# Kernel tuning notes

Measured on AMD Instinct MI355X. Metric: run time of the kernel, lower is better.

The kernel has to match this reference:

```python
import jax, jax.numpy as jnp
import numpy as np

DIM, DSTATE, DCONV, DTRANK = 192, 16, 4, 12
BSZ, HH, WW = 2, 64, 64
DW = DIM * 2  # SGFN dw_dim


def _silu(x):
    return x * jax.nn.sigmoid(x)


def _mamba(u, in_w, conv_w, conv_b, xproj_w, dt_w, dt_b, A_log, Dp, out_w):
    # u: [B, L, d_model]; d_inner == d_model (expand=1)
    Bb, L, d = u.shape
    xz = jnp.einsum('bld,ed->ble', u, in_w)            # [B,L,2d]
    xm, z = jnp.split(xz, 2, axis=-1)
    # causal depthwise conv1d (pad left d_conv-1, truncate to L)
    xt = xm.transpose(0, 2, 1)                          # [B,d,L]
    xt = jax.lax.conv_general_dilated(
        xt, conv_w[:, None, :], (1,), [(DCONV - 1, 0)],
        feature_group_count=d, dimension_numbers=('NCH', 'OIH', 'NCH'))
    xm = _silu((xt + conv_b[:, None]).transpose(0, 2, 1))  # [B,L,d]
    x_dbl = jnp.einsum('bld,ed->ble', xm, xproj_w)      # [B,L,r+2N]
    dt, Bm, Cm = jnp.split(x_dbl, [DTRANK, DTRANK + DSTATE], axis=-1)
    dt = jax.nn.softplus(jnp.einsum('blr,dr->bld', dt, dt_w) + dt_b)  # [B,L,d]
    A = -jnp.exp(A_log)                                 # [d,N]
    dA = jnp.exp(dt[..., None] * A)                     # [B,L,d,N]
    dBu = dt[..., None] * Bm[:, :, None, :] * xm[..., None]  # [B,L,d,N]

    def step(h, inp):
        a, bu, c = inp
        h = a * h + bu                                  # [B,d,N]
        return h, jnp.einsum('bdn,bn->bd', h, c)

    h0 = jnp.zeros((Bb, d, DSTATE), u.dtype)
    _, ys = jax.lax.scan(step, h0, (dA.swapaxes(0, 1), dBu.swapaxes(0, 1), Cm.swapaxes(0, 1)))
    y = ys.swapaxes(0, 1) + Dp * xm                     # [B,L,d]
    y = y * _silu(z)
    return jnp.einsum('bld,ed->ble', y, out_w)


def _forward(x, ln_w, ln_b,
             in_w0, conv_w0, conv_b0, xproj_w0, dt_w0, dt_b0, A_log0, D0, out_w0,
             in_w1, conv_w1, conv_b1, xproj_w1, dt_w1, dt_b1, A_log1, D1, out_w1,
             scale_mod, c1w, c1b, dww, dwb, c2w, c2b, gamma):
    Bb, C, Hh, Wh = x.shape
    # LayerNorm over channel dim (applied in BHWC layout)
    xn = x.transpose(0, 2, 3, 1)
    mu = xn.mean(-1, keepdims=True)
    var = ((xn - mu) ** 2).mean(-1, keepdims=True)
    xn = (xn - mu) * jax.lax.rsqrt(var + 1e-5) * ln_w + ln_b
    # MHSS: bidirectional Mamba over flattened spatial sequence
    xf = xn.reshape(Bb, Hh * Wh, C)
    out = _mamba(xf, in_w0, conv_w0, conv_b0, xproj_w0, dt_w0, dt_b0, A_log0, D0, out_w0)
    out = out + _mamba(xf[:, ::-1], in_w1, conv_w1, conv_b1, xproj_w1, dt_w1, dt_b1, A_log1, D1, out_w1)[:, ::-1]
    xm = out.reshape(Bb, Hh, Wh, C).transpose(0, 3, 1, 2) * scale_mod
    # SGFN
    t = jnp.einsum('bchw,oc->bohw', xm, c1w) + c1b[:, None, None]
    t = jax.lax.conv_general_dilated(
        t, dww, (1, 1), [(1, 1), (1, 1)],
        feature_group_count=dww.shape[0],
        dimension_numbers=('NCHW', 'OIHW', 'NCHW')) + dwb[:, None, None]
    t1, t2 = jnp.split(t, 2, axis=1)
    sg = jnp.einsum('bchw,oc->bohw', t1 * jax.nn.sigmoid(t2), c2w) + c2b[:, None, None]
    return x + gamma * (xm + sg)


def _mamba_params(key):
    ks = jax.random.split(key, 6)
    d, s = DIM, 0.02
    dt = jnp.exp(jax.random.uniform(ks[4], (d,), minval=np.log(1e-3), maxval=np.log(1e-1)))
    return dict(
        in_w=jax.random.normal(ks[0], (2 * d, d)) * s,
        conv_w=jax.random.normal(ks[1], (d, DCONV)) * s,
        conv_b=jnp.zeros((d,)),
        xproj_w=jax.random.normal(ks[2], (DTRANK + 2 * DSTATE, d)) * s,
        dt_w=jax.random.normal(ks[3], (d, DTRANK)) * (DTRANK ** -0.5),
        dt_b=jnp.log(jnp.expm1(dt)),  # inverse softplus
        A_log=jnp.log(jnp.tile(jnp.arange(1, DSTATE + 1, dtype=jnp.float32), (d, 1))),
        D=jnp.ones((d,)),
        out_w=jax.random.normal(ks[5], (d, d)) * s,
    )


def setup_inputs() -> dict:
    key = jax.random.key(0)
    ks = jax.random.split(key, 8)
    p0 = _mamba_params(ks[1])
    p1 = _mamba_params(ks[2])
    s = 0.02
    inp = {
        'x': jax.random.normal(ks[0], (BSZ, DIM, HH, WW), jnp.float32),
        'ln_w': jnp.ones((DIM,)),
        'ln_b': jnp.zeros((DIM,)),
        'scale_mod': jnp.full((1,), 0.25),
        'c1w': jax.random.normal(ks[3], (2 * DW, DIM)) * s,
        'c1b': jnp.zeros((2 * DW,)),
        'dww': jax.random.normal(ks[4], (2 * DW, 1, 3, 3)) * s,
        'dwb': jnp.zeros((2 * DW,)),
        'c2w': jax.random.normal(ks[5], (DIM, DW)) * s,
        'c2b': jnp.zeros((DIM,)),
        'gamma': jnp.full((1,), 0.1),  # nonzero so the block is non-trivial
    }
    for name, p in (('0', p0), ('1', p1)):
        inp['in_w' + name] = p['in_w']
        inp['conv_w' + name] = p['conv_w']
        inp['conv_b' + name] = p['conv_b']
        inp['xproj_w' + name] = p['xproj_w']
        inp['dt_w' + name] = p['dt_w']
        inp['dt_b' + name] = p['dt_b']
        inp['A_log' + name] = p['A_log']
        inp['D' + name] = p['D']
        inp['out_w' + name] = p['out_w']
    return inp


def reference(x, ln_w, ln_b,
              in_w0, conv_w0, conv_b0, xproj_w0, dt_w0, dt_b0, A_log0, D0, out_w0,
              in_w1, conv_w1, conv_b1, xproj_w1, dt_w1, dt_b1, A_log1, D1, out_w1,
              scale_mod, c1w, c1b, dww, dwb, c2w, c2b, gamma):
    return _forward(x, ln_w, ln_b,
                    in_w0, conv_w0, conv_b0, xproj_w0, dt_w0, dt_b0, A_log0, D0, out_w0,
                    in_w1, conv_w1, conv_b1, xproj_w1, dt_w1, dt_b1, A_log1, D1, out_w1,
                    scale_mod, c1w, c1b, dww, dwb, c2w, c2b, gamma)
```

## Files before the change

kernel.cpp:

```cpp
#include <hip/hip_runtime.h>
#include <hip/hip_bf16.h>

#define BSZ   2
#define SEQL  4096
#define BLR   8192
#define DM    192
#define NST   16
#define DTR   12
#define XDW   44
#define XDP   48
#define NCH   128
#define CT    32

typedef float f32x4 __attribute__((ext_vector_type(4)));
typedef __bf16 bf16x8 __attribute__((ext_vector_type(8)));
typedef __bf16 bf16x4 __attribute__((ext_vector_type(4)));

__device__ __forceinline__ float sigf(float x) { return 1.f / (1.f + __expf(-x)); }
__device__ __forceinline__ float siluf(float x) { return x * sigf(x); }
__device__ __forceinline__ float softplusf(float x) { return x > 20.f ? x : log1pf(__expf(x)); }

__global__ __launch_bounds__(256) void ln_kernel(const float* __restrict__ x,
                                                 const float* __restrict__ lw,
                                                 const float* __restrict__ lb,
                                                 __bf16* __restrict__ xn) {
    __shared__ float Xs[192][68];
    __shared__ float Rs[4][64], Rq[4][64];
    __shared__ float Mu[64], Rv[64];
    const int tid = threadIdx.x;
    const int blk = blockIdx.x;
    const int b = blk >> 6;
    const int hw0 = (blk & 63) << 6;
    {
        int i4 = tid & 15, cp = tid >> 4;
        for (int c = cp; c < 192; c += 16) {
            float4 v = *reinterpret_cast<const float4*>(x + ((size_t)b * DM + c) * 4096 + hw0 + i4 * 4);
            *reinterpret_cast<float4*>(&Xs[c][i4 * 4]) = v;
        }
    }
    __syncthreads();
    const int i = tid & 63, part = tid >> 6;
    float s = 0.f, q = 0.f;
    for (int c = part * 48; c < part * 48 + 48; c++) {
        float v = Xs[c][i];
        s += v; q += v * v;
    }
    Rs[part][i] = s; Rq[part][i] = q;
    __syncthreads();
    if (part == 0) {
        float ss = Rs[0][i] + Rs[1][i] + Rs[2][i] + Rs[3][i];
        float qq = Rq[0][i] + Rq[1][i] + Rq[2][i] + Rq[3][i];
        float mu = ss * (1.f / DM);
        float var = qq * (1.f / DM) - mu * mu;
        Mu[i] = mu; Rv[i] = rsqrtf(var + 1e-5f);
    }
    __syncthreads();
    float mu = Mu[i], rs = Rv[i];
    size_t rowb = ((size_t)b * 4096 + hw0 + i) * DM;
#pragma unroll
    for (int j = 0; j < 6; j++) {
        int c0 = part * 48 + j * 8;
        bf16x8 o;
#pragma unroll
        for (int e = 0; e < 8; e++) {
            int c = c0 + e;
            o[e] = (__bf16)((Xs[c][i] - mu) * rs * lw[c] + lb[c]);
        }
        *reinterpret_cast<bf16x8*>(xn + rowb + c0) = o;
    }
}

template <int EPI>
__global__ __launch_bounds__(256) void gemm_mfma(const __bf16* __restrict__ A, int lda,
                                                 const __bf16* __restrict__ W, int ldw,
                                                 __bf16* __restrict__ C, int ldc,
                                                 int N, int K,
                                                 const float* __restrict__ bias,
                                                 const float* __restrict__ scal,
                                                 const __bf16* __restrict__ aux,
                                                 const float* __restrict__ xres,
                                                 float* __restrict__ outp) {
    __shared__ __bf16 As[64][40];
    __shared__ __bf16 Ws[64][40];
    const int tid  = threadIdx.x;
    const int wave = tid >> 6, lane = tid & 63;
    const int ko = lane >> 4, lm = lane & 15;
    const int wm = (wave & 1) * 32, wn = (wave >> 1) * 32;
    const int m0 = blockIdx.y << 6;
    int n0 = blockIdx.x << 6;
    if (EPI == 5) {
        int dir = blockIdx.x;
        A += dir * DM;
        W += (size_t)dir * XDW * DM;
        C += (size_t)dir * BLR * XDP;
        n0 = 0;
    }
    const int r = tid >> 2, cq = (tid & 3) * 8;
    f32x4 acc[2][2] = {};

    for (int k0 = 0; k0 < K; k0 += 32) {
        {
            bf16x8 pk;
            const __bf16* ap = A + (size_t)(m0 + r) * lda + k0 + cq;
            if (k0 + cq + 8 <= K) pk = *reinterpret_cast<const bf16x8*>(ap);
            else {
#pragma unroll
                for (int j = 0; j < 8; j++) pk[j] = (k0 + cq + j < K) ? ap[j] : (__bf16)0.f;
            }
            *reinterpret_cast<bf16x8*>(&As[r][cq]) = pk;
        }
        {
            bf16x8 pk = {};
            if (n0 + r < N) {
                const __bf16* wp = W + (size_t)(n0 + r) * ldw + k0 + cq;
                if (k0 + cq + 8 <= K) pk = *reinterpret_cast<const bf16x8*>(wp);
                else {
#pragma unroll
                    for (int j = 0; j < 8; j++) pk[j] = (k0 + cq + j < K) ? wp[j] : (__bf16)0.f;
                }
            }
            *reinterpret_cast<bf16x8*>(&Ws[r][cq]) = pk;
        }
        __syncthreads();
        bf16x8 af[2], bfr[2];
#pragma unroll
        for (int ti = 0; ti < 2; ti++)
            af[ti] = *reinterpret_cast<bf16x8*>(&As[wm + ti * 16 + lm][ko * 8]);
#pragma unroll
        for (int tj = 0; tj < 2; tj++)
            bfr[tj] = *reinterpret_cast<bf16x8*>(&Ws[wn + tj * 16 + lm][ko * 8]);
#pragma unroll
        for (int ti = 0; ti < 2; ti++)
#pragma unroll
            for (int tj = 0; tj < 2; tj++)
                acc[ti][tj] = __builtin_amdgcn_mfma_f32_16x16x32_bf16(af[ti], bfr[tj], acc[ti][tj], 0, 0, 0);
        __syncthreads();
    }

    if constexpr (EPI == 4) {
        __shared__ float Cs[64][65];
#pragma unroll
        for (int ti = 0; ti < 2; ti++)
#pragma unroll
            for (int tj = 0; tj < 2; tj++) {
                int nn = n0 + wn + tj * 16 + lm;
#pragma unroll
                for (int reg = 0; reg < 4; reg++) {
                    int m = m0 + wm + ti * 16 + ko * 4 + reg;
                    float v = acc[ti][tj][reg];
                    if (nn < N) v += (float)aux[(size_t)m * DM + nn];
                    Cs[wm + ti * 16 + ko * 4 + reg][wn + tj * 16 + lm] = v;
                }
            }
        __syncthreads();
        float g = scal[0];
#pragma unroll
        for (int rep = 0; rep < 16; rep++) {
            int idx = rep * 256 + tid;
            int n = idx >> 6, mi = idx & 63;
            int nn = n0 + n;
            if (nn >= N) continue;
            int m = m0 + mi;
            int b = m >> 12, hw = m & 4095;
            size_t oi = (((size_t)b * DM + nn) << 12) + hw;
            outp[oi] = xres[oi] + g * (Cs[mi][n] + bias[nn]);
        }
        return;
    }

#pragma unroll
    for (int ti = 0; ti < 2; ti++)
#pragma unroll
        for (int tj = 0; tj < 2; tj++) {
            int n = n0 + wn + tj * 16 + lm;
            if (n >= N) continue;
#pragma unroll
            for (int reg = 0; reg < 4; reg++) {
                int m = m0 + wm + ti * 16 + ko * 4 + reg;
                float v = acc[ti][tj][reg];
                if (EPI == 1) v += bias[n];
                if (EPI == 3) v *= scal[0];
                C[(size_t)m * ldc + n] = (__bf16)v;
            }
        }
}

__global__ __launch_bounds__(256) void conv_silu_kernel(const __bf16* __restrict__ xz,
                                                        const float* __restrict__ cwt,
                                                        const float* __restrict__ cbcat,
                                                        __bf16* __restrict__ xc) {
    int idx = blockIdx.x * 256 + threadIdx.x;
    int colq = (idx % 48) << 3;
    int row = idx / 48;
    int dir = colq >= DM;
    int b = row >> 12, l = row & 4095;
    int xoff = colq + dir * DM;
    float acc[8];
    {
        float4 b0 = *reinterpret_cast<const float4*>(cbcat + colq);
        float4 b1 = *reinterpret_cast<const float4*>(cbcat + colq + 4);
        acc[0] = b0.x; acc[1] = b0.y; acc[2] = b0.z; acc[3] = b0.w;
        acc[4] = b1.x; acc[5] = b1.y; acc[6] = b1.z; acc[7] = b1.w;
    }
#pragma unroll
    for (int k = 0; k < 4; k++) {
        int ls = dir ? (l + 3 - k) : (l - 3 + k);
        if (ls < 0 || ls >= SEQL) continue;
        bf16x8 xv = *reinterpret_cast<const bf16x8*>(xz + ((size_t)(b << 12) + ls) * 768 + xoff);
        const float* wv = cwt + k * 384 + colq;
#pragma unroll
        for (int e = 0; e < 8; e++) acc[e] += wv[e] * (float)xv[e];
    }
    bf16x8 o;
#pragma unroll
    for (int e = 0; e < 8; e++) o[e] = (__bf16)siluf(acc[e]);
    *reinterpret_cast<bf16x8*>(xc + (size_t)row * 384 + colq) = o;
}

__global__ __launch_bounds__(192) void scan_partial(const __bf16* __restrict__ xcb,
                                                    const __bf16* __restrict__ xd,
                                                    const float* __restrict__ dtw0,
                                                    const float* __restrict__ dtw1,
                                                    const float* __restrict__ dtb0,
                                                    const float* __restrict__ dtb1,
                                                    const float* __restrict__ Alog0,
                                                    const float* __restrict__ Alog1,
                                                    float* __restrict__ S, float* __restrict__ P) {
    int d = threadIdx.x;
    int blk = blockIdx.x;
    int chunk = blk & (NCH - 1);
    int dirb = blk >> 7;
    int b = dirb >> 1, dir = dirb & 1;
    const float* Alog = dir ? Alog1 : Alog0;
    const float* dtw  = dir ? dtw1 : dtw0;
    float dtb = (dir ? dtb1 : dtb0)[d];
    float wdt[12];
#pragma unroll
    for (int r = 0; r < 12; r++) wdt[r] = dtw[d * DTR + r];
    float A[16], h[16];
#pragma unroll
    for (int n = 0; n < 16; n++) { A[n] = -__expf(Alog[d * NST + n]); h[n] = 0.f; }
    float sdt = 0.f;
    int col = dir * DM + d;
    const __bf16* xdd = xd + (size_t)dir * BLR * XDP;
    int l0 = chunk * CT;
    for (int s = 0; s < CT; s++) {
        int l = dir ? (SEQL - 1 - (l0 + s)) : (l0 + s);
        size_t row = ((size_t)b << 12) + l;
        const __bf16* xr = xdd + row * XDP;
        bf16x8 B0 = *reinterpret_cast<const bf16x8*>(xr);
        bf16x8 B1 = *reinterpret_cast<const bf16x8*>(xr + 8);
        bf16x8 R0 = *reinterpret_cast<const bf16x8*>(xr + 32);
        bf16x4 R1 = *reinterpret_cast<const bf16x4*>(xr + 40);
        float dtraw = dtb;
#pragma unroll
        for (int r = 0; r < 8; r++) dtraw += wdt[r] * (float)R0[r];
#pragma unroll
        for (int r = 0; r < 4; r++) dtraw += wdt[8 + r] * (float)R1[r];
        float dtv = softplusf(dtraw);
        float xcv = (float)xcb[row * 384 + col];
        float dx = dtv * xcv;
#pragma unroll
        for (int n = 0; n < 16; n++) {
            float Bv = (float)(n < 8 ? B0[n & 7] : B1[n & 7]);
            h[n] = __expf(dtv * A[n]) * h[n] + dx * Bv;
        }
        sdt += dtv;
    }
    float4* Sp = reinterpret_cast<float4*>(S + (size_t)blk * 3072 + d * 16);
    float4* Pp = reinterpret_cast<float4*>(P + (size_t)blk * 3072 + d * 16);
#pragma unroll
    for (int q = 0; q < 4; q++) {
        Sp[q] = make_float4(h[q * 4], h[q * 4 + 1], h[q * 4 + 2], h[q * 4 + 3]);
        Pp[q] = make_float4(__expf(A[q * 4] * sdt), __expf(A[q * 4 + 1] * sdt),
                            __expf(A[q * 4 + 2] * sdt), __expf(A[q * 4 + 3] * sdt));
    }
}

__global__ __launch_bounds__(256) void scan_combine(float* SH, const float* __restrict__ P) {
    int id = blockIdx.x * 256 + threadIdx.x;
    int dirb = id / 3072;
    int dn = id % 3072;
    float h = 0.f;
#pragma unroll 4
    for (int c = 0; c < NCH; c++) {
        size_t idx = (size_t)(dirb * NCH + c) * 3072 + dn;
        float s = SH[idx], p = P[idx];
        SH[idx] = h;
        h = p * h + s;
    }
}

__global__ __launch_bounds__(192) void scan_apply(const __bf16* __restrict__ xcb,
                                                  const __bf16* __restrict__ xd,
                                                  const __bf16* __restrict__ xzb,
                                                  const float* __restrict__ dtw0,
                                                  const float* __restrict__ dtw1,
                                                  const float* __restrict__ dtb0,
                                                  const float* __restrict__ dtb1,
                                                  const float* __restrict__ Alog0,
                                                  const float* __restrict__ Alog1,
                                                  const float* __restrict__ D0,
                                                  const float* __restrict__ D1,
                                                  const float* __restrict__ Hini,
                                                  __bf16* __restrict__ y) {
    int d = threadIdx.x;
    int blk = blockIdx.x;
    int chunk = blk & (NCH - 1);
    int dirb = blk >> 7;
    int b = dirb >> 1, dir = dirb & 1;
    const float* Alog = dir ? Alog1 : Alog0;
    const float* dtw  = dir ? dtw1 : dtw0;
    float dtb = (dir ? dtb1 : dtb0)[d];
    float Dv = (dir ? D1 : D0)[d];
    float wdt[12];
#pragma unroll
    for (int r = 0; r < 12; r++) wdt[r] = dtw[d * DTR + r];
    float A[16], h[16];
#pragma unroll
    for (int n = 0; n < 16; n++) A[n] = -__expf(Alog[d * NST + n]);
    const float4* Hp = reinterpret_cast<const float4*>(Hini + (size_t)blk * 3072 + d * 16);
#pragma unroll
    for (int q = 0; q < 4; q++) {
        float4 hq = Hp[q];
        h[q * 4] = hq.x; h[q * 4 + 1] = hq.y; h[q * 4 + 2] = hq.z; h[q * 4 + 3] = hq.w;
    }
    int col = dir * DM + d;
    const __bf16* xdd = xd + (size_t)dir * BLR * XDP;
    int l0 = chunk * CT;
    for (int s = 0; s < CT; s++) {
        int l = dir ? (SEQL - 1 - (l0 + s)) : (l0 + s);
        size_t row = ((size_t)b << 12) + l;
        const __bf16* xr = xdd + row * XDP;
        bf16x8 B0 = *reinterpret_cast<const bf16x8*>(xr);
        bf16x8 B1 = *reinterpret_cast<const bf16x8*>(xr + 8);
        bf16x8 C0 = *reinterpret_cast<const bf16x8*>(xr + 16);
        bf16x8 C1 = *reinterpret_cast<const bf16x8*>(xr + 24);
        bf16x8 R0 = *reinterpret_cast<const bf16x8*>(xr + 32);
        bf16x4 R1 = *reinterpret_cast<const bf16x4*>(xr + 40);
        float dtraw = dtb;
#pragma unroll
        for (int r = 0; r < 8; r++) dtraw += wdt[r] * (float)R0[r];
#pragma unroll
        for (int r = 0; r < 4; r++) dtraw += wdt[8 + r] * (float)R1[r];
        float dtv = softplusf(dtraw);
        float xcv = (float)xcb[row * 384 + col];
        float dx = dtv * xcv;
        float p = 0.f;
#pragma unroll
        for (int n = 0; n < 16; n++) {
            float Bv = (float)(n < 8 ? B0[n & 7] : B1[n & 7]);
            float Cv = (float)(n < 8 ? C0[n & 7] : C1[n & 7]);
            h[n] = __expf(dtv * A[n]) * h[n] + dx * Bv;
            p += h[n] * Cv;
        }
        float zv = (float)xzb[row * 768 + dir * 384 + DM + d];
        y[row * 384 + col] = (__bf16)((p + Dv * xcv) * siluf(zv));
    }
}

#define PK_WIN  (768 * 192)
#define PK_WCT  (192 * 384)
#define PK_XPW  (2 * XDW * 192)
#define PK_C1W  (768 * 192)
#define PK_C2W  (192 * 384)
#define PK_DWT  (9 * 768)
#define PK_CWT  (4 * 384)
#define PK_CB   384
#define PK_TOT  (PK_WIN + PK_WCT + PK_XPW + PK_C1W + PK_C2W + PK_DWT + PK_CWT + PK_CB)
__global__ void pack_weights(const float* __restrict__ iw0, const float* __restrict__ iw1,
                             const float* __restrict__ ow0, const float* __restrict__ ow1,
                             const float* __restrict__ xp0, const float* __restrict__ xp1,
                             const float* __restrict__ c1w, const float* __restrict__ c2w,
                             const float* __restrict__ dww,
                             const float* __restrict__ cw0, const float* __restrict__ cw1,
                             const float* __restrict__ cb0, const float* __restrict__ cb1,
                             __bf16* __restrict__ win, __bf16* __restrict__ wcat,
                             __bf16* __restrict__ xpw, __bf16* __restrict__ c1wb,
                             __bf16* __restrict__ c2wb,
                             float* __restrict__ dwt, float* __restrict__ cwt,
                             float* __restrict__ cbc) {
    int idx = blockIdx.x * 256 + threadIdx.x;
    int base = 0;
    if (idx < base + PK_WIN) {
        int j = idx - base;
        win[j] = (__bf16)((j < 384 * 192) ? iw0[j] : iw1[j - 384 * 192]);
        return;
    }
    base += PK_WIN;
    if (idx < base + PK_WCT) {
        int j = idx - base;
        int n = j / 384, k = j % 384;
        wcat[j] = (__bf16)((k < DM) ? ow0[n * DM + k] : ow1[n * DM + k - DM]);
        return;
    }
    base += PK_WCT;
    if (idx < base + PK_XPW) {
        int j = idx - base;
        int dir = j / (XDW * 192);
        int rem = j - dir * (XDW * 192);
        int np = rem / 192, k = rem % 192;
        int src = (np < 32) ? (np + DTR) : (np - 32);
        xpw[j] = (__bf16)((dir ? xp1 : xp0)[src * 192 + k]);
        return;
    }
    base += PK_XPW;
    if (idx < base + PK_C1W) {
        int j = idx - base;
        c1wb[j] = (__bf16)c1w[j];
        return;
    }
    base += PK_C1W;
    if (idx < base + PK_C2W) {
        int j = idx - base;
        c2wb[j] = (__bf16)c2w[j];
        return;
    }
    base += PK_C2W;
    if (idx < base + PK_DWT) {
        int j = idx - base;
        int wi = j / 768, c = j % 768;
        dwt[j] = dww[c * 9 + wi];
        return;
    }
    base += PK_DWT;
    if (idx < base + PK_CWT) {
        int j = idx - base;
        int k = j / 384, col = j % 384;
        int dir = col >= DM, d = col - dir * DM;
        cwt[j] = (dir ? cw1 : cw0)[d * 4 + k];
        return;
    }
    base += PK_CWT;
    if (idx < base + PK_CB) {
        int col = idx - base;
        int dir = col >= DM, d = col - dir * DM;
        cbc[col] = (dir ? cb1 : cb0)[d];
    }
}

__global__ __launch_bounds__(256) void dwgate_kernel(const __bf16* __restrict__ t,
                                                     const float* __restrict__ dwt,
                                                     const float* __restrict__ dwb,
                                                     __bf16* __restrict__ g) {
    int idx = blockIdx.x * 256 + threadIdx.x;
    int jq = (idx % 48) << 3;
    int row = idx / 48;
    int b = row >> 12, hw = row & 4095;
    int h = hw >> 6, w = hw & 63;
    float a1[8], a2[8];
    {
        float4 x0 = *reinterpret_cast<const float4*>(dwb + jq);
        float4 x1 = *reinterpret_cast<const float4*>(dwb + jq + 4);
        float4 y0 = *reinterpret_cast<const float4*>(dwb + 384 + jq);
        float4 y1 = *reinterpret_cast<const float4*>(dwb + 384 + jq + 4);
        a1[0]=x0.x;a1[1]=x0.y;a1[2]=x0.z;a1[3]=x0.w;a1[4]=x1.x;a1[5]=x1.y;a1[6]=x1.z;a1[7]=x1.w;
        a2[0]=y0.x;a2[1]=y0.y;a2[2]=y0.z;a2[3]=y0.w;a2[4]=y1.x;a2[5]=y1.y;a2[6]=y1.z;a2[7]=y1.w;
    }
#pragma unroll
    for (int dy = -1; dy <= 1; dy++) {
        int hh = h + dy;
        if (hh < 0 || hh >= 64) continue;
#pragma unroll
        for (int dx = -1; dx <= 1; dx++) {
            int ww = w + dx;
            if (ww < 0 || ww >= 64) continue;
            size_t base = ((size_t)(b << 12) + (hh << 6) + ww) * 768;
            int wi = (dy + 1) * 3 + (dx + 1);
            bf16x8 t1 = *reinterpret_cast<const bf16x8*>(t + base + jq);
            bf16x8 t2 = *reinterpret_cast<const bf16x8*>(t + base + 384 + jq);
            const float* w1 = dwt + wi * 768 + jq;
            const float* w2 = dwt + wi * 768 + 384 + jq;
#pragma unroll
            for (int e = 0; e < 8; e++) {
                a1[e] += w1[e] * (float)t1[e];
                a2[e] += w2[e] * (float)t2[e];
            }
        }
    }
    bf16x8 o;
#pragma unroll
    for (int e = 0; e < 8; e++) o[e] = (__bf16)(a1[e] * sigf(a2[e]));
    *reinterpret_cast<bf16x8*>(g + (size_t)row * 384 + jq) = o;
}

extern "C" void kernel_launch(void* const* d_in, const int* in_sizes, int n_in,
                              void* d_out, int out_size, void* d_ws, size_t ws_size,
                              hipStream_t stream) {
    const float* x         = (const float*)d_in[0];
    const float* ln_w      = (const float*)d_in[1];
    const float* ln_b      = (const float*)d_in[2];
    const float* scale_mod = (const float*)d_in[3];
    const float* c1w       = (const float*)d_in[4];
    const float* c1b       = (const float*)d_in[5];
    const float* dww       = (const float*)d_in[6];
    const float* dwb       = (const float*)d_in[7];
    const float* c2w       = (const float*)d_in[8];
    const float* c2b       = (const float*)d_in[9];
    const float* gamma     = (const float*)d_in[10];
    const float* in_w0     = (const float*)d_in[11];
    const float* conv_w0   = (const float*)d_in[12];
    const float* conv_b0   = (const float*)d_in[13];
    const float* xproj_w0  = (const float*)d_in[14];
    const float* dt_w0     = (const float*)d_in[15];
    const float* dt_b0     = (const float*)d_in[16];
    const float* A_log0    = (const float*)d_in[17];
    const float* D0        = (const float*)d_in[18];
    const float* out_w0    = (const float*)d_in[19];
    const float* in_w1     = (const float*)d_in[20];
    const float* conv_w1   = (const float*)d_in[21];
    const float* conv_b1   = (const float*)d_in[22];
    const float* xproj_w1  = (const float*)d_in[23];
    const float* dt_w1     = (const float*)d_in[24];
    const float* dt_b1     = (const float*)d_in[25];
    const float* A_log1    = (const float*)d_in[26];
    const float* D1        = (const float*)d_in[27];
    const float* out_w1    = (const float*)d_in[28];

    char* wsb = (char*)d_ws;
    size_t off = 0;
    auto alloc = [&](size_t bytes) { size_t o = off; off += (bytes + 255) & ~(size_t)255; return o; };
    const size_t o_xn   = alloc((size_t)BLR * DM * 2);
    const size_t o_xz   = alloc((size_t)BLR * 768 * 2);
    const size_t o_xc   = alloc((size_t)BLR * 384 * 2);
    const size_t o_y    = alloc((size_t)BLR * 384 * 2);
    const size_t o_xm   = alloc((size_t)BLR * DM * 2);
    const size_t o_xd   = alloc((size_t)2 * BLR * XDP * 2);
    const size_t o_S    = alloc((size_t)4 * NCH * 3072 * 4);
    const size_t o_P    = alloc((size_t)4 * NCH * 3072 * 4);
    const size_t o_win  = alloc((size_t)PK_WIN * 2);
    const size_t o_wct  = alloc((size_t)PK_WCT * 2);
    const size_t o_xpw  = alloc((size_t)PK_XPW * 2);
    const size_t o_c1w  = alloc((size_t)PK_C1W * 2);
    const size_t o_c2w  = alloc((size_t)PK_C2W * 2);
    const size_t o_dwt  = alloc((size_t)PK_DWT * 4);
    const size_t o_cwt  = alloc((size_t)PK_CWT * 4);
    const size_t o_cb   = alloc((size_t)PK_CB * 4);

    __bf16* xn  = (__bf16*)(wsb + o_xn);
    __bf16* xz  = (__bf16*)(wsb + o_xz);
    __bf16* xc  = (__bf16*)(wsb + o_xc);
    __bf16* yb  = (__bf16*)(wsb + o_y);
    __bf16* xm  = (__bf16*)(wsb + o_xm);
    __bf16* xd  = (__bf16*)(wsb + o_xd);
    float*  Sb  = (float*)(wsb + o_S);
    float*  Pb  = (float*)(wsb + o_P);
    __bf16* win = (__bf16*)(wsb + o_win);
    __bf16* wct = (__bf16*)(wsb + o_wct);
    __bf16* xpw = (__bf16*)(wsb + o_xpw);
    __bf16* c1wb= (__bf16*)(wsb + o_c1w);
    __bf16* c2wb= (__bf16*)(wsb + o_c2w);
    float*  dwt = (float*)(wsb + o_dwt);
    float*  cwt = (float*)(wsb + o_cwt);
    float*  cbc = (float*)(wsb + o_cb);

    ln_kernel<<<128, 256, 0, stream>>>(x, ln_w, ln_b, xn);
    pack_weights<<<(PK_TOT + 255) / 256, 256, 0, stream>>>(in_w0, in_w1, out_w0, out_w1,
                                                           xproj_w0, xproj_w1, c1w, c2w,
                                                           dww, conv_w0, conv_w1, conv_b0, conv_b1,
                                                           win, wct, xpw, c1wb, c2wb, dwt, cwt, cbc);
    gemm_mfma<0><<<dim3(12, 128), 256, 0, stream>>>(xn, DM, win, DM, xz, 768, 768, DM,
                                                    nullptr, nullptr, nullptr, nullptr, nullptr);
    conv_silu_kernel<<<(BLR * 48) / 256, 256, 0, stream>>>(xz, cwt, cbc, xc);
    gemm_mfma<5><<<dim3(2, 128), 256, 0, stream>>>(xc, 384, xpw, DM, xd, XDP, XDW, DM,
                                                   nullptr, nullptr, nullptr, nullptr, nullptr);
    scan_partial<<<4 * NCH, 192, 0, stream>>>(xc, xd, dt_w0, dt_w1, dt_b0, dt_b1,
                                              A_log0, A_log1, Sb, Pb);
    scan_combine<<<48, 256, 0, stream>>>(Sb, Pb);
    scan_apply<<<4 * NCH, 192, 0, stream>>>(xc, xd, xz, dt_w0, dt_w1, dt_b0, dt_b1,
                                            A_log0, A_log1, D0, D1, Sb, yb);
    gemm_mfma<3><<<dim3(3, 128), 256, 0, stream>>>(yb, 384, wct, 384, xm, DM, DM, 384,
                                                   nullptr, scale_mod, nullptr, nullptr, nullptr);
    gemm_mfma<1><<<dim3(12, 128), 256, 0, stream>>>(xm, DM, c1wb, DM, xz, 768, 768, DM,
                                                    c1b, nullptr, nullptr, nullptr, nullptr);
    dwgate_kernel<<<(BLR * 48) / 256, 256, 0, stream>>>(xz, dwt, dwb, xc);
    gemm_mfma<4><<<dim3(3, 128), 256, 0, stream>>>(xc, 384, c2wb, 384, nullptr, 0, DM, 384,
                                                   c2b, gamma, xm, x, (float*)d_out);
}
```

Baseline: 289.7 us.

## Fuse LN with weight packing, widen GEMM K-tile, split scan state across thread pairs

LayerNorm and weight packing now run in one launch, and LayerNorm uses smaller 32-row tiles so there are more blocks. The GEMM K-step grows from 32 to 64, with two MFMA sub-steps per LDS load, which halves the number of barriers. The bounds checks on K are dropped, which assumes K is a multiple of 64; both K=192 and K=384 are. The scan kernels split the 16 SSM states across two threads per channel, doubling thread count for more latency hiding, and pay for it with a shuffle reduction for the C·h dot product.

```diff
diff --git a/kernel.cpp b/kernel.cpp
--- a/kernel.cpp
+++ b/kernel.cpp
@@ -20,36 +20,113 @@
 __device__ __forceinline__ float siluf(float x) { return x * sigf(x); }
 __device__ __forceinline__ float softplusf(float x) { return x > 20.f ? x : log1pf(__expf(x)); }
 
-__global__ __launch_bounds__(256) void ln_kernel(const float* __restrict__ x,
-                                                 const float* __restrict__ lw,
-                                                 const float* __restrict__ lb,
-                                                 __bf16* __restrict__ xn) {
-    __shared__ float Xs[192][68];
-    __shared__ float Rs[4][64], Rq[4][64];
-    __shared__ float Mu[64], Rv[64];
+#define PK_WIN  (768 * 192)
+#define PK_WCT  (192 * 384)
+#define PK_XPW  (2 * XDW * 192)
+#define PK_C1W  (768 * 192)
+#define PK_C2W  (192 * 384)
+#define PK_DWT  (9 * 768)
+#define PK_CWT  (4 * 384)
+#define PK_CB   384
+#define PK_TOT  (PK_WIN + PK_WCT + PK_XPW + PK_C1W + PK_C2W + PK_DWT + PK_CWT + PK_CB)
+#define LN_BLOCKS 256
+#define PK_BLOCKS ((PK_TOT + 255) / 256)
+
+__global__ __launch_bounds__(256) void ln_pack_kernel(const float* __restrict__ x,
+                                                      const float* __restrict__ lw,
+                                                      const float* __restrict__ lb,
+                                                      __bf16* __restrict__ xn,
+                                                      const float* __restrict__ iw0, const float* __restrict__ iw1,
+                                                      const float* __restrict__ ow0, const float* __restrict__ ow1,
+                                                      const float* __restrict__ xp0, const float* __restrict__ xp1,
+                                                      const float* __restrict__ c1w, const float* __restrict__ c2w,
+                                                      const float* __restrict__ dww,
+                                                      const float* __restrict__ cw0, const float* __restrict__ cw1,
+                                                      const float* __restrict__ cb0, const float* __restrict__ cb1,
+                                                      __bf16* __restrict__ win, __bf16* __restrict__ wcat,
+                                                      __bf16* __restrict__ xpw, __bf16* __restrict__ c1wb,
+                                                      __bf16* __restrict__ c2wb,
+                                                      float* __restrict__ dwt, float* __restrict__ cwt,
+                                                      float* __restrict__ cbc) {
     const int tid = threadIdx.x;
+    if (blockIdx.x >= LN_BLOCKS) {
+        int idx = (blockIdx.x - LN_BLOCKS) * 256 + tid;
+        int base = 0;
+        if (idx < base + PK_WIN) {
+            int j = idx - base;
+            win[j] = (__bf16)((j < 384 * 192) ? iw0[j] : iw1[j - 384 * 192]);
+            return;
+        }
+        base += PK_WIN;
+        if (idx < base + PK_WCT) {
+            int j = idx - base;
+            int n = j / 384, k = j % 384;
+            wcat[j] = (__bf16)((k < DM) ? ow0[n * DM + k] : ow1[n * DM + k - DM]);
+            return;
+        }
+        base += PK_WCT;
+        if (idx < base + PK_XPW) {
+            int j = idx - base;
+            int dir = j / (XDW * 192);
+            int rem = j - dir * (XDW * 192);
+            int np = rem / 192, k = rem % 192;
+            int src = (np < 32) ? (np + DTR) : (np - 32);
+            xpw[j] = (__bf16)((dir ? xp1 : xp0)[src * 192 + k]);
+            return;
+        }
+        base += PK_XPW;
+        if (idx < base + PK_C1W) { c1wb[idx - base] = (__bf16)c1w[idx - base]; return; }
+        base += PK_C1W;
+        if (idx < base + PK_C2W) { c2wb[idx - base] = (__bf16)c2w[idx - base]; return; }
+        base += PK_C2W;
+        if (idx < base + PK_DWT) {
+            int j = idx - base;
+            int wi = j / 768, c = j % 768;
+            dwt[j] = dww[c * 9 + wi];
+            return;
+        }
+        base += PK_DWT;
+        if (idx < base + PK_CWT) {
+            int j = idx - base;
+            int k = j / 384, col = j % 384;
+            int dir = col >= DM, d = col - dir * DM;
+            cwt[j] = (dir ? cw1 : cw0)[d * 4 + k];
+            return;
+        }
+        base += PK_CWT;
+        if (idx < base + PK_CB) {
+            int col = idx - base;
+            int dir = col >= DM, d = col - dir * DM;
+            cbc[col] = (dir ? cb1 : cb0)[d];
+        }
+        return;
+    }
+    __shared__ float Xs[192][36];
+    __shared__ float Rs[8][32], Rq[8][32];
+    __shared__ float Mu[32], Rv[32];
     const int blk = blockIdx.x;
-    const int b = blk >> 6;
-    const int hw0 = (blk & 63) << 6;
+    const int b = blk >> 7;
+    const int hw0 = (blk & 127) << 5;
     {
-        int i4 = tid & 15, cp = tid >> 4;
-        for (int c = cp; c < 192; c += 16) {
+        int i4 = tid & 7, cp = tid >> 3;
+        for (int c = cp; c < 192; c += 32) {
             float4 v = *reinterpret_cast<const float4*>(x + ((size_t)b * DM + c) * 4096 + hw0 + i4 * 4);
             *reinterpret_cast<float4*>(&Xs[c][i4 * 4]) = v;
         }
     }
     __syncthreads();
-    const int i = tid & 63, part = tid >> 6;
+    const int i = tid & 31, part = tid >> 5;
     float s = 0.f, q = 0.f;
-    for (int c = part * 48; c < part * 48 + 48; c++) {
+    for (int c = part * 24; c < part * 24 + 24; c++) {
         float v = Xs[c][i];
         s += v; q += v * v;
     }
     Rs[part][i] = s; Rq[part][i] = q;
     __syncthreads();
     if (part == 0) {
-        float ss = Rs[0][i] + Rs[1][i] + Rs[2][i] + Rs[3][i];
-        float qq = Rq[0][i] + Rq[1][i] + Rq[2][i] + Rq[3][i];
+        float ss = 0.f, qq = 0.f;
+#pragma unroll
+        for (int p = 0; p < 8; p++) { ss += Rs[p][i]; qq += Rq[p][i]; }
         float mu = ss * (1.f / DM);
         float var = qq * (1.f / DM) - mu * mu;
         Mu[i] = mu; Rv[i] = rsqrtf(var + 1e-5f);
@@ -58,8 +135,8 @@
     float mu = Mu[i], rs = Rv[i];
     size_t rowb = ((size_t)b * 4096 + hw0 + i) * DM;
 #pragma unroll
-    for (int j = 0; j < 6; j++) {
-        int c0 = part * 48 + j * 8;
+    for (int j = 0; j < 3; j++) {
+        int c0 = part * 24 + j * 8;
         bf16x8 o;
 #pragma unroll
         for (int e = 0; e < 8; e++) {
@@ -80,8 +157,8 @@
                                                  const __bf16* __restrict__ aux,
                                                  const float* __restrict__ xres,
                                                  float* __restrict__ outp) {
-    __shared__ __bf16 As[64][40];
-    __shared__ __bf16 Ws[64][40];
+    __shared__ __bf16 As[64][72];
+    __shared__ __bf16 Ws[64][72];
     const int tid  = threadIdx.x;
     const int wave = tid >> 6, lane = tid & 63;
     const int ko = lane >> 4, lm = lane & 15;
@@ -95,45 +172,41 @@
         C += (size_t)dir * BLR * XDP;
         n0 = 0;
     }
-    const int r = tid >> 2, cq = (tid & 3) * 8;
+    const int r = tid >> 2, cq = (tid & 3) * 16;
     f32x4 acc[2][2] = {};
 
-    for (int k0 = 0; k0 < K; k0 += 32) {
+    for (int k0 = 0; k0 < K; k0 += 64) {
         {
-            bf16x8 pk;
             const __bf16* ap = A + (size_t)(m0 + r) * lda + k0 + cq;
-            if (k0 + cq + 8 <= K) pk = *reinterpret_cast<const bf16x8*>(ap);
-            else {
-#pragma unroll
-                for (int j = 0; j < 8; j++) pk[j] = (k0 + cq + j < K) ? ap[j] : (__bf16)0.f;
-            }
-            *reinterpret_cast<bf16x8*>(&As[r][cq]) = pk;
+            *reinterpret_cast<bf16x8*>(&As[r][cq])     = *reinterpret_cast<const bf16x8*>(ap);
+            *reinterpret_cast<bf16x8*>(&As[r][cq + 8]) = *reinterpret_cast<const bf16x8*>(ap + 8);
         }
         {
-            bf16x8 pk = {};
+            bf16x8 w0 = {}, w1 = {};
             if (n0 + r < N) {
                 const __bf16* wp = W + (size_t)(n0 + r) * ldw + k0 + cq;
-                if (k0 + cq + 8 <= K) pk = *reinterpret_cast<const bf16x8*>(wp);
-                else {
-#pragma unroll
-                    for (int j = 0; j < 8; j++) pk[j] = (k0 + cq + j < K) ? wp[j] : (__bf16)0.f;
-                }
+                w0 = *reinterpret_cast<const bf16x8*>(wp);
+                w1 = *reinterpret_cast<const bf16x8*>(wp + 8);
             }
-            *reinterpret_cast<bf16x8*>(&Ws[r][cq]) = pk;
+            *reinterpret_cast<bf16x8*>(&Ws[r][cq])     = w0;
+            *reinterpret_cast<bf16x8*>(&Ws[r][cq + 8]) = w1;
         }
         __syncthreads();
-        bf16x8 af[2], bfr[2];
-#pragma unroll
-        for (int ti = 0; ti < 2; ti++)
-            af[ti] = *reinterpret_cast<bf16x8*>(&As[wm + ti * 16 + lm][ko * 8]);
-#pragma unroll
-        for (int tj = 0; tj < 2; tj++)
-            bfr[tj] = *reinterpret_cast<bf16x8*>(&Ws[wn + tj * 16 + lm][ko * 8]);
-#pragma unroll
-        for (int ti = 0; ti < 2; ti++)
+#pragma unroll
+        for (int kb = 0; kb < 2; kb++) {
+            bf16x8 af[2], bfr[2];
+#pragma unroll
+            for (int ti = 0; ti < 2; ti++)
+                af[ti] = *reinterpret_cast<bf16x8*>(&As[wm + ti * 16 + lm][kb * 32 + ko * 8]);
 #pragma unroll
             for (int tj = 0; tj < 2; tj++)
-                acc[ti][tj] = __builtin_amdgcn_mfma_f32_16x16x32_bf16(af[ti], bfr[tj], acc[ti][tj], 0, 0, 0);
+                bfr[tj] = *reinterpret_cast<bf16x8*>(&Ws[wn + tj * 16 + lm][kb * 32 + ko * 8]);
+#pragma unroll
+            for (int ti = 0; ti < 2; ti++)
+#pragma unroll
+                for (int tj = 0; tj < 2; tj++)
+                    acc[ti][tj] = __builtin_amdgcn_mfma_f32_16x16x32_bf16(af[ti], bfr[tj], acc[ti][tj], 0, 0, 0);
+        }
         __syncthreads();
     }
 
@@ -217,7 +290,7 @@
     *reinterpret_cast<bf16x8*>(xc + (size_t)row * 384 + colq) = o;
 }
 
-__global__ __launch_bounds__(192) void scan_partial(const __bf16* __restrict__ xcb,
+__global__ __launch_bounds__(384) void scan_partial(const __bf16* __restrict__ xcb,
                                                     const __bf16* __restrict__ xd,
                                                     const float* __restrict__ dtw0,
                                                     const float* __restrict__ dtw1,
@@ -226,7 +299,8 @@
                                                     const float* __restrict__ Alog0,
                                                     const float* __restrict__ Alog1,
                                                     float* __restrict__ S, float* __restrict__ P) {
-    int d = threadIdx.x;
+    int tid = threadIdx.x;
+    int d = tid >> 1, half = tid & 1;
     int blk = blockIdx.x;
     int chunk = blk & (NCH - 1);
     int dirb = blk >> 7;
@@ -237,9 +311,9 @@
     float wdt[12];
 #pragma unroll
     for (int r = 0; r < 12; r++) wdt[r] = dtw[d * DTR + r];
-    float A[16], h[16];
-#pragma unroll
-    for (int n = 0; n < 16; n++) { A[n] = -__expf(Alog[d * NST + n]); h[n] = 0.f; }
+    float A[8], h[8];
+#pragma unroll
+    for (int n = 0; n < 8; n++) { A[n] = -__expf(Alog[d * NST + half * 8 + n]); h[n] = 0.f; }
     float sdt = 0.f;
     int col = dir * DM + d;
     const __bf16* xdd = xd + (size_t)dir * BLR * XDP;
@@ -248,8 +322,7 @@
         int l = dir ? (SEQL - 1 - (l0 + s)) : (l0 + s);
         size_t row = ((size_t)b << 12) + l;
         const __bf16* xr = xdd + row * XDP;
-        bf16x8 B0 = *reinterpret_cast<const bf16x8*>(xr);
-        bf16x8 B1 = *reinterpret_cast<const bf16x8*>(xr + 8);
+        bf16x8 Bv = *reinterpret_cast<const bf16x8*>(xr + half * 8);
         bf16x8 R0 = *reinterpret_cast<const bf16x8*>(xr + 32);
         bf16x4 R1 = *reinterpret_cast<const bf16x4*>(xr + 40);
         float dtraw = dtb;
@@ -261,19 +334,19 @@
         float xcv = (float)xcb[row * 384 + col];
         float dx = dtv * xcv;
 #pragma unroll
-        for (int n = 0; n < 16; n++) {
-            float Bv = (float)(n < 8 ? B0[n & 7] : B1[n & 7]);
-            h[n] = __expf(dtv * A[n]) * h[n] + dx * Bv;
-        }
+        for (int n = 0; n < 8; n++)
+            h[n] = __expf(dtv * A[n]) * h[n] + dx * (float)Bv[n];
         sdt += dtv;
     }
-    float4* Sp = reinterpret_cast<float4*>(S + (size_t)blk * 3072 + d * 16);
-    float4* Pp = reinterpret_cast<float4*>(P + (size_t)blk * 3072 + d * 16);
-#pragma unroll
-    for (int q = 0; q < 4; q++) {
-        Sp[q] = make_float4(h[q * 4], h[q * 4 + 1], h[q * 4 + 2], h[q * 4 + 3]);
-        Pp[q] = make_float4(__expf(A[q * 4] * sdt), __expf(A[q * 4 + 1] * sdt),
-                            __expf(A[q * 4 + 2] * sdt), __expf(A[q * 4 + 3] * sdt));
+    float* Sp = S + (size_t)blk * 3072 + d * 16 + half * 8;
+    float* Pp = P + (size_t)blk * 3072 + d * 16 + half * 8;
+#pragma unroll
+    for (int q = 0; q < 2; q++) {
+        *reinterpret_cast<float4*>(Sp + q * 4) =
+            make_float4(h[q * 4], h[q * 4 + 1], h[q * 4 + 2], h[q * 4 + 3]);
+        *reinterpret_cast<float4*>(Pp + q * 4) =
+            make_float4(__expf(A[q * 4] * sdt), __expf(A[q * 4 + 1] * sdt),
+                        __expf(A[q * 4 + 2] * sdt), __expf(A[q * 4 + 3] * sdt));
     }
 }
 
@@ -291,7 +364,7 @@
     }
 }
 
-__global__ __launch_bounds__(192) void scan_apply(const __bf16* __restrict__ xcb,
+__global__ __launch_bounds__(384) void scan_apply(const __bf16* __restrict__ xcb,
                                                   const __bf16* __restrict__ xd,
                                                   const __bf16* __restrict__ xzb,
                                                   const float* __restrict__ dtw0,
@@ -304,7 +377,8 @@
                                                   const float* __restrict__ D1,
                                                   const float* __restrict__ Hini,
                                                   __bf16* __restrict__ y) {
-    int d = threadIdx.x;
+    int tid = threadIdx.x;
+    int d = tid >> 1, half = tid & 1;
     int blk = blockIdx.x;
     int chunk = blk & (NCH - 1);
     int dirb = blk >> 7;
@@ -316,14 +390,15 @@
     float wdt[12];
 #pragma unroll
     for (int r = 0; r < 12; r++) wdt[r] = dtw[d * DTR + r];
-    float A[16], h[16];
-#pragma unroll
-    for (int n = 0; n < 16; n++) A[n] = -__expf(Alog[d * NST + n]);
-    const float4* Hp = reinterpret_cast<const float4*>(Hini + (size_t)blk * 3072 + d * 16);
-#pragma unroll
-    for (int q = 0; q < 4; q++) {
-        float4 hq = Hp[q];
-        h[q * 4] = hq.x; h[q * 4 + 1] = hq.y; h[q * 4 + 2] = hq.z; h[q * 4 + 3] = hq.w;
+    float A[8], h[8];
+#pragma unroll
+    for (int n = 0; n < 8; n++) A[n] = -__expf(Alog[d * NST + half * 8 + n]);
+    {
+        const float* Hp = Hini + (size_t)blk * 3072 + d * 16 + half * 8;
+        float4 h0 = *reinterpret_cast<const float4*>(Hp);
+        float4 h1 = *reinterpret_cast<const float4*>(Hp + 4);
+        h[0] = h0.x; h[1] = h0.y; h[2] = h0.z; h[3] = h0.w;
+        h[4] = h1.x; h[5] = h1.y; h[6] = h1.z; h[7] = h1.w;
     }
     int col = dir * DM + d;
     const __bf16* xdd = xd + (size_t)dir * BLR * XDP;
@@ -332,10 +407,8 @@
         int l = dir ? (SEQL - 1 - (l0 + s)) : (l0 + s);
         size_t row = ((size_t)b << 12) + l;
         const __bf16* xr = xdd + row * XDP;
-        bf16x8 B0 = *reinterpret_cast<const bf16x8*>(xr);
-        bf16x8 B1 = *reinterpret_cast<const bf16x8*>(xr + 8);
-        bf16x8 C0 = *reinterpret_cast<const bf16x8*>(xr + 16);
-        bf16x8 C1 = *reinterpret_cast<const bf16x8*>(xr + 24);
+        bf16x8 Bv = *reinterpret_cast<const bf16x8*>(xr + half * 8);
+        bf16x8 Cv = *reinterpret_cast<const bf16x8*>(xr + 16 + half * 8);
         bf16x8 R0 = *reinterpret_cast<const bf16x8*>(xr + 32);
         bf16x4 R1 = *reinterpret_cast<const bf16x4*>(xr + 40);
         float dtraw = dtb;
@@ -348,94 +421,15 @@
         float dx = dtv * xcv;
         float p = 0.f;
 #pragma unroll
-        for (int n = 0; n < 16; n++) {
-            float Bv = (float)(n < 8 ? B0[n & 7] : B1[n & 7]);
-            float Cv = (float)(n < 8 ? C0[n & 7] : C1[n & 7]);
-            h[n] = __expf(dtv * A[n]) * h[n] + dx * Bv;
-            p += h[n] * Cv;
-        }
-        float zv = (float)xzb[row * 768 + dir * 384 + DM + d];
-        y[row * 384 + col] = (__bf16)((p + Dv * xcv) * siluf(zv));
-    }
-}
-
-#define PK_WIN  (768 * 192)
-#define PK_WCT  (192 * 384)
-#define PK_XPW  (2 * XDW * 192)
-#define PK_C1W  (768 * 192)
-#define PK_C2W  (192 * 384)
-#define PK_DWT  (9 * 768)
-#define PK_CWT  (4 * 384)
-#define PK_CB   384
-#define PK_TOT  (PK_WIN + PK_WCT + PK_XPW + PK_C1W + PK_C2W + PK_DWT + PK_CWT + PK_CB)
-__global__ void pack_weights(const float* __restrict__ iw0, const float* __restrict__ iw1,
-                             const float* __restrict__ ow0, const float* __restrict__ ow1,
-                             const float* __restrict__ xp0, const float* __restrict__ xp1,
-                             const float* __restrict__ c1w, const float* __restrict__ c2w,
-                             const float* __restrict__ dww,
-                             const float* __restrict__ cw0, const float* __restrict__ cw1,
-                             const float* __restrict__ cb0, const float* __restrict__ cb1,
-                             __bf16* __restrict__ win, __bf16* __restrict__ wcat,
-                             __bf16* __restrict__ xpw, __bf16* __restrict__ c1wb,
-                             __bf16* __restrict__ c2wb,
-                             float* __restrict__ dwt, float* __restrict__ cwt,
-                             float* __restrict__ cbc) {
-    int idx = blockIdx.x * 256 + threadIdx.x;
-    int base = 0;
-    if (idx < base + PK_WIN) {
-        int j = idx - base;
-        win[j] = (__bf16)((j < 384 * 192) ? iw0[j] : iw1[j - 384 * 192]);
-        return;
-    }
-    base += PK_WIN;
-    if (idx < base + PK_WCT) {
-        int j = idx - base;
-        int n = j / 384, k = j % 384;
-        wcat[j] = (__bf16)((k < DM) ? ow0[n * DM + k] : ow1[n * DM + k - DM]);
-        return;
-    }
-    base += PK_WCT;
-    if (idx < base + PK_XPW) {
-        int j = idx - base;
-        int dir = j / (XDW * 192);
-        int rem = j - dir * (XDW * 192);
-        int np = rem / 192, k = rem % 192;
-        int src = (np < 32) ? (np + DTR) : (np - 32);
-        xpw[j] = (__bf16)((dir ? xp1 : xp0)[src * 192 + k]);
-        return;
-    }
-    base += PK_XPW;
-    if (idx < base + PK_C1W) {
-        int j = idx - base;
-        c1wb[j] = (__bf16)c1w[j];
-        return;
-    }
-    base += PK_C1W;
-    if (idx < base + PK_C2W) {
-        int j = idx - base;
-        c2wb[j] = (__bf16)c2w[j];
-        return;
-    }
-    base += PK_C2W;
-    if (idx < base + PK_DWT) {
-        int j = idx - base;
-        int wi = j / 768, c = j % 768;
-        dwt[j] = dww[c * 9 + wi];
-        return;
-    }
-    base += PK_DWT;
-    if (idx < base + PK_CWT) {
-        int j = idx - base;
-        int k = j / 384, col = j % 384;
-        int dir = col >= DM, d = col - dir * DM;
-        cwt[j] = (dir ? cw1 : cw0)[d * 4 + k];
-        return;
-    }
-    base += PK_CWT;
-    if (idx < base + PK_CB) {
-        int col = idx - base;
-        int dir = col >= DM, d = col - dir * DM;
-        cbc[col] = (dir ? cb1 : cb0)[d];
+        for (int n = 0; n < 8; n++) {
+            h[n] = __expf(dtv * A[n]) * h[n] + dx * (float)Bv[n];
+            p += h[n] * (float)Cv[n];
+        }
+        p += __shfl_xor(p, 1);
+        if (half == 0) {
+            float zv = (float)xzb[row * 768 + dir * 384 + DM + d];
+            y[row * 384 + col] = (__bf16)((p + Dv * xcv) * siluf(zv));
+        }
     }
 }
 
@@ -554,20 +548,20 @@
     float*  cwt = (float*)(wsb + o_cwt);
     float*  cbc = (float*)(wsb + o_cb);
 
-    ln_kernel<<<128, 256, 0, stream>>>(x, ln_w, ln_b, xn);
-    pack_weights<<<(PK_TOT + 255) / 256, 256, 0, stream>>>(in_w0, in_w1, out_w0, out_w1,
-                                                           xproj_w0, xproj_w1, c1w, c2w,
-                                                           dww, conv_w0, conv_w1, conv_b0, conv_b1,
-                                                           win, wct, xpw, c1wb, c2wb, dwt, cwt, cbc);
+    ln_pack_kernel<<<LN_BLOCKS + PK_BLOCKS, 256, 0, stream>>>(
+        x, ln_w, ln_b, xn,
+        in_w0, in_w1, out_w0, out_w1, xproj_w0, xproj_w1, c1w, c2w,
+        dww, conv_w0, conv_w1, conv_b0, conv_b1,
+        win, wct, xpw, c1wb, c2wb, dwt, cwt, cbc);
     gemm_mfma<0><<<dim3(12, 128), 256, 0, stream>>>(xn, DM, win, DM, xz, 768, 768, DM,
                                                     nullptr, nullptr, nullptr, nullptr, nullptr);
     conv_silu_kernel<<<(BLR * 48) / 256, 256, 0, stream>>>(xz, cwt, cbc, xc);
     gemm_mfma<5><<<dim3(2, 128), 256, 0, stream>>>(xc, 384, xpw, DM, xd, XDP, XDW, DM,
                                                    nullptr, nullptr, nullptr, nullptr, nullptr);
-    scan_partial<<<4 * NCH, 192, 0, stream>>>(xc, xd, dt_w0, dt_w1, dt_b0, dt_b1,
+    scan_partial<<<4 * NCH, 384, 0, stream>>>(xc, xd, dt_w0, dt_w1, dt_b0, dt_b1,
                                               A_log0, A_log1, Sb, Pb);
     scan_combine<<<48, 256, 0, stream>>>(Sb, Pb);
-    scan_apply<<<4 * NCH, 192, 0, stream>>>(xc, xd, xz, dt_w0, dt_w1, dt_b0, dt_b1,
+    scan_apply<<<4 * NCH, 384, 0, stream>>>(xc, xd, xz, dt_w0, dt_w1, dt_b0, dt_b1,
                                             A_log0, A_log1, D0, D1, Sb, yb);
     gemm_mfma<3><<<dim3(3, 128), 256, 0, stream>>>(yb, 384, wct, 384, xm, DM, DM, 384,
                                                    nullptr, scale_mod, nullptr, nullptr, nullptr);
```

Result: slower. 306.5 us (+5.8%).
